# Performance work log

Measured on AMD Instinct MI355X. Metric: run time of the kernel, lower is better.

The kernel has to match this reference:

```python
import jax, jax.numpy as jnp
import numpy as np

B, S, D = 4, 2048, 512
H, DK, DV = 8, 64, 64


def setup_inputs() -> dict:
    key = jax.random.key(0)
    ks = jax.random.split(key, 9)
    inp = {
        "input_Q": jax.random.normal(ks[0], (B, S, D), dtype=jnp.float32),
        "input_K": jax.random.normal(ks[1], (B, S, D), dtype=jnp.float32),
        "input_V": jax.random.normal(ks[2], (B, S, D), dtype=jnp.float32),
        "attn_mask": jax.random.bernoulli(ks[3], 0.1, (B, S, S)),
        "other": jax.random.normal(ks[4], (B, S, S), dtype=jnp.float32),
        # nn.Linear weights stored [out_features, in_features]
        "W_Q": jax.random.normal(ks[5], (H * DK, D), dtype=jnp.float32) * (1.0 / np.sqrt(D)),
        "W_K": jax.random.normal(ks[6], (H * DK, D), dtype=jnp.float32) * (1.0 / np.sqrt(D)),
        "W_V": jax.random.normal(ks[7], (H * DV, D), dtype=jnp.float32) * (1.0 / np.sqrt(D)),
        "W_fc": jax.random.normal(ks[8], (D, H * DV), dtype=jnp.float32) * (1.0 / np.sqrt(H * DV)),
    }
    return inp


def reference(input_Q, input_K, input_V, attn_mask, other, W_Q, W_K, W_V, W_fc):
    b, s, _ = input_Q.shape
    # projections: y = x @ W.T, then split heads -> [B,H,S,dk]
    Q = (input_Q @ W_Q.T).reshape(b, s, H, DK).transpose(0, 2, 1, 3)
    K = (input_K @ W_K.T).reshape(b, s, H, DK).transpose(0, 2, 1, 3)
    V = (input_V @ W_V.T).reshape(b, s, H, DV).transpose(0, 2, 1, 3)
    scale = 1.0 / np.sqrt(DK).astype(np.float32)
    scores = jnp.einsum("bhqd,bhkd->bhqk", Q, K) * scale  # [B,H,S,S]
    scores = scores + other[:, None, :, :]  # additive bias broadcast over heads
    scores = jnp.where(attn_mask[:, None, :, :], jnp.float32(-1e9), scores)
    attn = jax.nn.softmax(scores, axis=-1)
    context = jnp.einsum("bhqk,bhkd->bhqd", attn, V)  # [B,H,S,DV]
    context = context.transpose(0, 2, 1, 3).reshape(b, s, H * DV)
    output = context @ W_fc.T  # dropout is identity at inference
    return (output, attn)
```

## Files before the change

kernel.cpp:

```cpp
#include <hip/hip_runtime.h>

#define BB 4
#define SS 2048
#define DDIM 512
#define HH 8
#define MTOK (BB*SS)
#define BHN (BB*HH)

typedef _Float16 f16;
typedef __attribute__((ext_vector_type(8))) _Float16 half8;
typedef __attribute__((ext_vector_type(4))) _Float16 half4;
typedef __attribute__((ext_vector_type(4))) float float4v;
typedef __attribute__((ext_vector_type(4))) int int4v;

#define SCALE_L2E 0.180336880073616f
#define L2E 1.44269504088896f
#define EBIAS 4.0f
#define MASKVAL -65504.0f

__device__ __forceinline__ float4v mfma_k32(half8 a, half8 b, float4v c) {
  return __builtin_amdgcn_mfma_f32_16x16x32_f16(a, b, c, 0, 0, 0);
}

__device__ __forceinline__ half8 cvt8(float4v a, float4v b) {
  half8 r;
  r[0] = (f16)a[0]; r[1] = (f16)a[1]; r[2] = (f16)a[2]; r[3] = (f16)a[3];
  r[4] = (f16)b[0]; r[5] = (f16)b[1]; r[6] = (f16)b[2]; r[7] = (f16)b[3];
  return r;
}

__global__ __launch_bounds__(256) void detect_mask_kernel(
    const unsigned int* __restrict__ m, unsigned int* __restrict__ flag) {
  unsigned int v = 0;
  const int base = blockIdx.x * 1024;
  for (int j = threadIdx.x; j < 1024; j += 256)
    if (m[base + j] > 1u) v = 1u;
  if (v) atomicOr(flag, 1u);
}

__global__ __launch_bounds__(256) void gemm_qkv(
    const float* __restrict__ inQ, const float* __restrict__ inK,
    const float* __restrict__ inV, const float* __restrict__ WQ,
    const float* __restrict__ WK, const float* __restrict__ WV,
    f16* __restrict__ Qp, f16* __restrict__ Kfrag, f16* __restrict__ Vfrag) {
  __shared__ f16 As[128][40];
  __shared__ f16 Bs[128][40];
  const int z = blockIdx.z;
  const float* A = (z == 0) ? inQ : (z == 1) ? inK : inV;
  const float* W = (z == 0) ? WQ : (z == 1) ? WK : WV;
  const int t = threadIdx.x;
  const int bm = blockIdx.x * 128;
  const int bn = blockIdx.y * 128;
  const int w = t >> 6, ln = t & 63;
  const int wr = w >> 1, wc = w & 1;
  const int lr = ln & 15, lg = ln >> 4;
  const int srow = t >> 1, scol = (t & 1) * 16;

  float4v acc[4][4] = {};

  for (int k0 = 0; k0 < 512; k0 += 32) {
    {
      const float* ap = A + (size_t)(bm + srow) * 512 + k0 + scol;
      float4v x0 = *(const float4v*)ap,       x1 = *(const float4v*)(ap + 4);
      float4v x2 = *(const float4v*)(ap + 8), x3 = *(const float4v*)(ap + 12);
      *(half8*)&As[srow][scol]     = cvt8(x0, x1);
      *(half8*)&As[srow][scol + 8] = cvt8(x2, x3);
    }
    {
      const float* wp = W + (size_t)(bn + srow) * 512 + k0 + scol;
      float4v x0 = *(const float4v*)wp,       x1 = *(const float4v*)(wp + 4);
      float4v x2 = *(const float4v*)(wp + 8), x3 = *(const float4v*)(wp + 12);
      *(half8*)&Bs[srow][scol]     = cvt8(x0, x1);
      *(half8*)&Bs[srow][scol + 8] = cvt8(x2, x3);
    }
    __syncthreads();
    half8 af[4], bf[4];
    #pragma unroll
    for (int m = 0; m < 4; m++) af[m] = *(const half8*)&As[wr * 64 + m * 16 + lr][lg * 8];
    #pragma unroll
    for (int n = 0; n < 4; n++) bf[n] = *(const half8*)&Bs[wc * 64 + n * 16 + lr][lg * 8];
    #pragma unroll
    for (int m = 0; m < 4; m++)
      #pragma unroll
      for (int n = 0; n < 4; n++) acc[m][n] = mfma_k32(af[m], bf[n], acc[m][n]);
    __syncthreads();
  }

  #pragma unroll
  for (int m = 0; m < 4; m++) {
    int row = bm + wr * 64 + m * 16 + lg * 4;
    #pragma unroll
    for (int n = 0; n < 4; n++) {
      int col = bn + wc * 64 + n * 16 + lr;
      int b_ = row >> 11, s_ = row & 2047, h_ = col >> 6, d_ = col & 63;
      if (z == 0) {
        #pragma unroll
        for (int r = 0; r < 4; r++)
          Qp[(size_t)(row + r) * 512 + col] = (f16)acc[m][n][r];
      } else if (z == 1) {
        #pragma unroll
        for (int r = 0; r < 4; r++) {
          int tok = s_ + r;
          Kfrag[((((size_t)(b_ * 8 + h_)) * 128 + (tok >> 4)) * 2 + (d_ >> 5)) * 512 +
                ((tok & 15) + 16 * ((d_ >> 3) & 3)) * 8 + (d_ & 7)] =
              (f16)acc[m][n][r];
        }
      } else {
        half4 ph;
        ph[0] = (f16)acc[m][n][0]; ph[1] = (f16)acc[m][n][1];
        ph[2] = (f16)acc[m][n][2]; ph[3] = (f16)acc[m][n][3];
        *(half4*)&Vfrag[((((size_t)(b_ * 8 + h_)) * 64 + (s_ >> 5)) * 4 + (d_ >> 4)) * 512 +
                        ((d_ & 15) + 16 * ((s_ >> 2) & 3)) * 8 + ((s_ >> 2) & 4)] = ph;
      }
    }
  }
}

__global__ __launch_bounds__(256) void gemm_out(const f16* __restrict__ ctx2,
                                                const float* __restrict__ W,
                                                float* __restrict__ Out) {
  __shared__ f16 As[128][40];
  __shared__ f16 Bs[128][40];
  const int t = threadIdx.x;
  const int bm = blockIdx.x * 128;
  const int bn = blockIdx.y * 128;
  const int w = t >> 6, ln = t & 63;
  const int wr = w >> 1, wc = w & 1;
  const int lr = ln & 15, lg = ln >> 4;
  const int srow = t >> 1, scol = (t & 1) * 16;

  float4v acc[4][4] = {};

  for (int k0 = 0; k0 < 512; k0 += 32) {
    {
      const f16* ap = ctx2 + (size_t)(bm + srow) * 512 + k0 + scol;
      const f16* ap2 = ap + (size_t)MTOK * 512;
      half8 x0 = *(const half8*)(ap),  x1 = *(const half8*)(ap + 8);
      half8 y0 = *(const half8*)(ap2), y1 = *(const half8*)(ap2 + 8);
      *(half8*)&As[srow][scol]     = x0 + y0;
      *(half8*)&As[srow][scol + 8] = x1 + y1;
    }
    {
      const float* wp = W + (size_t)(bn + srow) * 512 + k0 + scol;
      float4v x0 = *(const float4v*)wp,       x1 = *(const float4v*)(wp + 4);
      float4v x2 = *(const float4v*)(wp + 8), x3 = *(const float4v*)(wp + 12);
      *(half8*)&Bs[srow][scol]     = cvt8(x0, x1);
      *(half8*)&Bs[srow][scol + 8] = cvt8(x2, x3);
    }
    __syncthreads();
    half8 af[4], bf[4];
    #pragma unroll
    for (int m = 0; m < 4; m++) af[m] = *(const half8*)&As[wr * 64 + m * 16 + lr][lg * 8];
    #pragma unroll
    for (int n = 0; n < 4; n++) bf[n] = *(const half8*)&Bs[wc * 64 + n * 16 + lr][lg * 8];
    #pragma unroll
    for (int m = 0; m < 4; m++)
      #pragma unroll
      for (int n = 0; n < 4; n++) acc[m][n] = mfma_k32(af[m], bf[n], acc[m][n]);
    __syncthreads();
  }

  #pragma unroll
  for (int m = 0; m < 4; m++) {
    int row = bm + wr * 64 + m * 16 + lg * 4;
    #pragma unroll
    for (int n = 0; n < 4; n++) {
      int col = bn + wc * 64 + n * 16 + lr;
      #pragma unroll
      for (int r = 0; r < 4; r++)
        Out[(size_t)(row + r) * 512 + col] = acc[m][n][r];
    }
  }
}

#define LOADK(dst, st) {                                        \
    const f16* p_ = kfb + (size_t)(st) * 2048;                  \
    dst##0 = *(const half8*)(p_);                               \
    dst##1 = *(const half8*)(p_ + 512);                         \
    dst##2 = *(const half8*)(p_ + 1024);                        \
    dst##3 = *(const half8*)(p_ + 1536); }
#define LOADV(dst, st) {                                        \
    const f16* p_ = vfb + (size_t)(st) * 2048;                  \
    dst##0 = *(const half8*)(p_);                               \
    dst##1 = *(const half8*)(p_ + 512);                         \
    dst##2 = *(const half8*)(p_ + 1024);                        \
    dst##3 = *(const half8*)(p_ + 1536); }

template<int PHASE>
__global__ __launch_bounds__(512, (PHASE == 1) ? 6 : 4) void attn_pass(
    const f16* __restrict__ Qp, const f16* __restrict__ Kfrag,
    const f16* __restrict__ Vfrag, const float* __restrict__ other,
    const unsigned char* __restrict__ mask8, const int* __restrict__ mask32,
    const unsigned int* __restrict__ flag, float* __restrict__ lsum2,
    float* __restrict__ attn_out, f16* __restrict__ ctx2) {
  __shared__ f16 othm[16][1032];

  const int t = threadIdx.x;
  const int bid = blockIdx.x;
  const int b  = (bid >> 1) & 3;
  const int kh = bid & 1;
  const int qblk = (bid >> 3) * 16;
  const int w = t >> 6, ln = t & 63;
  const int lr = ln & 15, lg = ln >> 4;
  const bool use8 = (*flag) != 0;

  {
    const int q = t >> 5, k0 = (t & 31) * 32;
    const size_t base = ((size_t)b * SS + qblk + q) * SS + kh * 1024 + k0;
    const float* op = other + base;
    if (use8) {
      const unsigned char* mp = mask8 + base;
      #pragma unroll
      for (int g = 0; g < 4; g++) {
        unsigned int mw0 = *(const unsigned int*)(mp + g * 8);
        unsigned int mw1 = *(const unsigned int*)(mp + g * 8 + 4);
        float4v o0 = *(const float4v*)(op + g * 8);
        float4v o1 = *(const float4v*)(op + g * 8 + 4);
        float4v r0, r1;
        #pragma unroll
        for (int r = 0; r < 4; r++) {
          r0[r] = ((mw0 >> (8 * r)) & 0xffu) ? MASKVAL : fmaf(o0[r], L2E, -EBIAS);
          r1[r] = ((mw1 >> (8 * r)) & 0xffu) ? MASKVAL : fmaf(o1[r], L2E, -EBIAS);
        }
        *(half8*)&othm[q][k0 + g * 8] = cvt8(r0, r1);
      }
    } else {
      const int* mp = mask32 + base;
      #pragma unroll
      for (int g = 0; g < 4; g++) {
        int4v m0 = *(const int4v*)(mp + g * 8);
        int4v m1 = *(const int4v*)(mp + g * 8 + 4);
        float4v o0 = *(const float4v*)(op + g * 8);
        float4v o1 = *(const float4v*)(op + g * 8 + 4);
        float4v r0, r1;
        #pragma unroll
        for (int r = 0; r < 4; r++) {
          r0[r] = m0[r] ? MASKVAL : fmaf(o0[r], L2E, -EBIAS);
          r1[r] = m1[r] ? MASKVAL : fmaf(o1[r], L2E, -EBIAS);
        }
        *(half8*)&othm[q][k0 + g * 8] = cvt8(r0, r1);
      }
    }
  }
  __syncthreads();

  const int h = w, bh = b * 8 + h;
  const f16* qp = Qp + ((size_t)b * SS + qblk + lr) * 512 + h * 64 + lg * 8;
  const half8 qf0 = *(const half8*)qp;
  const half8 qf1 = *(const half8*)(qp + 32);

  float invl = 0.f;
  if (PHASE == 2) {
    const size_t qi = (size_t)bh * SS + qblk + lr;
    invl = 1.0f / (lsum2[qi] + lsum2[(size_t)BHN * SS + qi]);
  }

  float rs = 0.f;
  float4v cacc0 = {}, cacc1 = {}, cacc2 = {}, cacc3 = {};

  const f16* kfb = Kfrag + ((size_t)bh * 128 + kh * 64) * 2 * 512 + ln * 8;
  const f16* vfb = Vfrag + ((size_t)bh * 64 + kh * 32) * 4 * 512 + ln * 8;
  float* abase = attn_out + ((size_t)bh * SS + qblk + lr) * SS + kh * 1024;

  half8 kA0, kA1, kA2, kA3, kB0, kB1, kB2, kB3;
  half8 vA0, vA1, vA2, vA3, vB0, vB1, vB2, vB3;

  LOADK(kA, 0);
  if (PHASE == 2) LOADV(vA, 0);

  #define BODY(kf, vf, st) {                                              \
    const int stn = ((st) < 31) ? (st) + 1 : 31;                          \
    (void)stn;                                                            \
    float4v s0 = {}, s1 = {};                                             \
    s0 = mfma_k32(kf##0, qf0, s0);                                        \
    s0 = mfma_k32(kf##1, qf1, s0);                                        \
    s1 = mfma_k32(kf##2, qf0, s1);                                        \
    s1 = mfma_k32(kf##3, qf1, s1);                                        \
    const int kl = (st) * 32;                                             \
    const half4 o40 = *(const half4*)&othm[lr][kl + lg * 4];              \
    const half4 o41 = *(const half4*)&othm[lr][kl + 16 + lg * 4];         \
    float4v ev0, ev1;                                                     \
    _Pragma("unroll")                                                     \
    for (int r = 0; r < 4; r++) {                                         \
      ev0[r] = exp2f(fmaf(s0[r], SCALE_L2E, (float)o40[r]));              \
      ev1[r] = exp2f(fmaf(s1[r], SCALE_L2E, (float)o41[r]));              \
    }                                                                     \
    if (PHASE == 1) {                                                     \
      rs += (ev0[0] + ev0[1]) + (ev0[2] + ev0[3]) +                       \
            (ev1[0] + ev1[1]) + (ev1[2] + ev1[3]);                        \
    } else {                                                              \
      float4v av0 = ev0 * invl, av1 = ev1 * invl;                         \
      *(float4v*)(abase + kl + lg * 4) = av0;                             \
      *(float4v*)(abase + kl + 16 + lg * 4) = av1;                        \
      half8 pa8 = cvt8(av0, av1);                                         \
      cacc0 = mfma_k32(pa8, vf##0, cacc0);                                \
      cacc1 = mfma_k32(pa8, vf##1, cacc1);                                \
      cacc2 = mfma_k32(pa8, vf##2, cacc2);                                \
      cacc3 = mfma_k32(pa8, vf##3, cacc3);                                \
    }                                                                     \
  }

  for (int st2 = 0; st2 < 16; st2++) {
    const int se = st2 * 2;
    {
      const int stn = (se < 31) ? se + 1 : 31;
      LOADK(kB, stn);
      if (PHASE == 2) LOADV(vB, stn);
      BODY(kA, vA, se);
    }
    {
      const int so = se + 1;
      const int stn = (so < 31) ? so + 1 : 31;
      LOADK(kA, stn);
      if (PHASE == 2) LOADV(vA, stn);
      BODY(kB, vB, so);
    }
  }
  #undef BODY

  if (PHASE == 1) {
    float v = rs;
    v += __shfl_xor(v, 16);
    v += __shfl_xor(v, 32);
    if (ln < 16)
      lsum2[(size_t)kh * BHN * SS + (size_t)bh * SS + qblk + lr] = v;
  } else {
    #pragma unroll
    for (int r = 0; r < 4; r++) {
      const size_t crow = (size_t)kh * MTOK * 512 +
                          ((size_t)b * SS + qblk + lg * 4 + r) * 512 + h * 64;
      ctx2[crow + 0 * 16 + lr] = (f16)cacc0[r];
      ctx2[crow + 1 * 16 + lr] = (f16)cacc1[r];
      ctx2[crow + 2 * 16 + lr] = (f16)cacc2[r];
      ctx2[crow + 3 * 16 + lr] = (f16)cacc3[r];
    }
  }
}

extern "C" void kernel_launch(void* const* d_in, const int* in_sizes, int n_in,
                              void* d_out, int out_size, void* d_ws, size_t ws_size,
                              hipStream_t stream) {
  const float* inQ   = (const float*)d_in[0];
  const float* inK   = (const float*)d_in[1];
  const float* inV   = (const float*)d_in[2];
  const void*  mask  = d_in[3];
  const float* other = (const float*)d_in[4];
  const float* WQ    = (const float*)d_in[5];
  const float* WK    = (const float*)d_in[6];
  const float* WV    = (const float*)d_in[7];
  const float* WF    = (const float*)d_in[8];

  char* ws = (char*)d_ws;
  size_t off = 0;
  unsigned int* flag = (unsigned int*)(ws + off); off += 256;
  f16* Qp    = (f16*)(ws + off); off += (size_t)MTOK * 512 * 2;
  f16* Kfrag = (f16*)(ws + off); off += (size_t)MTOK * 512 * 2;
  f16* Vfrag = (f16*)(ws + off); off += (size_t)MTOK * 512 * 2;
  float* lsum2 = (float*)(ws + off); off += (size_t)2 * BHN * SS * 4;
  f16* ctx2  = (f16*)(ws + off); off += (size_t)2 * MTOK * 512 * 2;
  if (ws_size < off) return;

  float* outp  = (float*)d_out;
  float* attnp = outp + (size_t)MTOK * DDIM;

  hipMemsetAsync(flag, 0, 256, stream);
  detect_mask_kernel<<<64, 256, 0, stream>>>((const unsigned int*)mask, flag);

  gemm_qkv<<<dim3(64, 4, 3), 256, 0, stream>>>(inQ, inK, inV, WQ, WK, WV,
                                               Qp, Kfrag, Vfrag);

  attn_pass<1><<<1024, 512, 0, stream>>>(
      Qp, Kfrag, Vfrag, other, (const unsigned char*)mask, (const int*)mask,
      flag, lsum2, attnp, ctx2);
  attn_pass<2><<<1024, 512, 0, stream>>>(
      Qp, Kfrag, Vfrag, other, (const unsigned char*)mask, (const int*)mask,
      flag, lsum2, attnp, ctx2);

  gemm_out<<<dim3(64, 4), 256, 0, stream>>>(ctx2, WF, outp);
}
```

Baseline: 377.5 us.

## Fuse two attention passes into one kernel covering full key range per block

Replaces the two-launch attention scheme (a row-sum pass and a normalize+PV pass, each split across two key halves) with a single kernel in which each block handles all 2048 keys for a 16-query tile. The block computes the row sum and then recomputes the scores for normalization and the PV product. This removes the second read and preprocessing of the mask/bias into shared memory, the lsum2 workspace, and the half-summed ctx2 buffer that gemm_out had to add. In exchange the grid halves to 512 blocks, shared memory per block doubles, and occupancy drops (launch bounds 512,2), which may reduce latency hiding.

```diff
diff --git a/kernel.cpp b/kernel.cpp
--- a/kernel.cpp
+++ b/kernel.cpp
@@ -116,7 +116,7 @@
   }
 }
 
-__global__ __launch_bounds__(256) void gemm_out(const f16* __restrict__ ctx2,
+__global__ __launch_bounds__(256) void gemm_out(const f16* __restrict__ ctx,
                                                 const float* __restrict__ W,
                                                 float* __restrict__ Out) {
   __shared__ f16 As[128][40];
@@ -133,12 +133,9 @@
 
   for (int k0 = 0; k0 < 512; k0 += 32) {
     {
-      const f16* ap = ctx2 + (size_t)(bm + srow) * 512 + k0 + scol;
-      const f16* ap2 = ap + (size_t)MTOK * 512;
-      half8 x0 = *(const half8*)(ap),  x1 = *(const half8*)(ap + 8);
-      half8 y0 = *(const half8*)(ap2), y1 = *(const half8*)(ap2 + 8);
-      *(half8*)&As[srow][scol]     = x0 + y0;
-      *(half8*)&As[srow][scol + 8] = x1 + y1;
+      const f16* ap = ctx + (size_t)(bm + srow) * 512 + k0 + scol;
+      *(half8*)&As[srow][scol]     = *(const half8*)(ap);
+      *(half8*)&As[srow][scol + 8] = *(const half8*)(ap + 8);
     }
     {
       const float* wp = W + (size_t)(bn + srow) * 512 + k0 + scol;
@@ -186,32 +183,30 @@
     dst##2 = *(const half8*)(p_ + 1024);                        \
     dst##3 = *(const half8*)(p_ + 1536); }
 
-template<int PHASE>
-__global__ __launch_bounds__(512, (PHASE == 1) ? 6 : 4) void attn_pass(
+__global__ __launch_bounds__(512, 2) void attn_fused(
     const f16* __restrict__ Qp, const f16* __restrict__ Kfrag,
     const f16* __restrict__ Vfrag, const float* __restrict__ other,
     const unsigned char* __restrict__ mask8, const int* __restrict__ mask32,
-    const unsigned int* __restrict__ flag, float* __restrict__ lsum2,
-    float* __restrict__ attn_out, f16* __restrict__ ctx2) {
-  __shared__ f16 othm[16][1032];
+    const unsigned int* __restrict__ flag, float* __restrict__ attn_out,
+    f16* __restrict__ ctx) {
+  __shared__ f16 othm[16][2056];
 
   const int t = threadIdx.x;
   const int bid = blockIdx.x;
-  const int b  = (bid >> 1) & 3;
-  const int kh = bid & 1;
-  const int qblk = (bid >> 3) * 16;
+  const int b = bid & 3;
+  const int qblk = (bid >> 2) * 16;
   const int w = t >> 6, ln = t & 63;
   const int lr = ln & 15, lg = ln >> 4;
   const bool use8 = (*flag) != 0;
 
   {
-    const int q = t >> 5, k0 = (t & 31) * 32;
-    const size_t base = ((size_t)b * SS + qblk + q) * SS + kh * 1024 + k0;
+    const int q = t >> 5, k0 = (t & 31) * 64;
+    const size_t base = ((size_t)b * SS + qblk + q) * SS + k0;
     const float* op = other + base;
     if (use8) {
       const unsigned char* mp = mask8 + base;
       #pragma unroll
-      for (int g = 0; g < 4; g++) {
+      for (int g = 0; g < 8; g++) {
         unsigned int mw0 = *(const unsigned int*)(mp + g * 8);
         unsigned int mw1 = *(const unsigned int*)(mp + g * 8 + 4);
         float4v o0 = *(const float4v*)(op + g * 8);
@@ -227,7 +222,7 @@
     } else {
       const int* mp = mask32 + base;
       #pragma unroll
-      for (int g = 0; g < 4; g++) {
+      for (int g = 0; g < 8; g++) {
         int4v m0 = *(const int4v*)(mp + g * 8);
         int4v m1 = *(const int4v*)(mp + g * 8 + 4);
         float4v o0 = *(const float4v*)(op + g * 8);
@@ -249,28 +244,17 @@
   const half8 qf0 = *(const half8*)qp;
   const half8 qf1 = *(const half8*)(qp + 32);
 
-  float invl = 0.f;
-  if (PHASE == 2) {
-    const size_t qi = (size_t)bh * SS + qblk + lr;
-    invl = 1.0f / (lsum2[qi] + lsum2[(size_t)BHN * SS + qi]);
-  }
-
-  float rs = 0.f;
-  float4v cacc0 = {}, cacc1 = {}, cacc2 = {}, cacc3 = {};
-
-  const f16* kfb = Kfrag + ((size_t)bh * 128 + kh * 64) * 2 * 512 + ln * 8;
-  const f16* vfb = Vfrag + ((size_t)bh * 64 + kh * 32) * 4 * 512 + ln * 8;
-  float* abase = attn_out + ((size_t)bh * SS + qblk + lr) * SS + kh * 1024;
+  const f16* kfb = Kfrag + (size_t)bh * 128 * 2 * 512 + ln * 8;
+  const f16* vfb = Vfrag + (size_t)bh * 64 * 4 * 512 + ln * 8;
+  float* abase = attn_out + ((size_t)bh * SS + qblk + lr) * SS;
 
   half8 kA0, kA1, kA2, kA3, kB0, kB1, kB2, kB3;
   half8 vA0, vA1, vA2, vA3, vB0, vB1, vB2, vB3;
 
+  float rs = 0.f;
   LOADK(kA, 0);
-  if (PHASE == 2) LOADV(vA, 0);
-
-  #define BODY(kf, vf, st) {                                              \
-    const int stn = ((st) < 31) ? (st) + 1 : 31;                          \
-    (void)stn;                                                            \
+
+  #define BODYA(kf, st) {                                                 \
     float4v s0 = {}, s1 = {};                                             \
     s0 = mfma_k32(kf##0, qf0, s0);                                        \
     s0 = mfma_k32(kf##1, qf1, s0);                                        \
@@ -285,55 +269,82 @@
       ev0[r] = exp2f(fmaf(s0[r], SCALE_L2E, (float)o40[r]));              \
       ev1[r] = exp2f(fmaf(s1[r], SCALE_L2E, (float)o41[r]));              \
     }                                                                     \
-    if (PHASE == 1) {                                                     \
-      rs += (ev0[0] + ev0[1]) + (ev0[2] + ev0[3]) +                       \
-            (ev1[0] + ev1[1]) + (ev1[2] + ev1[3]);                        \
-    } else {                                                              \
-      float4v av0 = ev0 * invl, av1 = ev1 * invl;                         \
-      *(float4v*)(abase + kl + lg * 4) = av0;                             \
-      *(float4v*)(abase + kl + 16 + lg * 4) = av1;                        \
-      half8 pa8 = cvt8(av0, av1);                                         \
-      cacc0 = mfma_k32(pa8, vf##0, cacc0);                                \
-      cacc1 = mfma_k32(pa8, vf##1, cacc1);                                \
-      cacc2 = mfma_k32(pa8, vf##2, cacc2);                                \
-      cacc3 = mfma_k32(pa8, vf##3, cacc3);                                \
+    rs += (ev0[0] + ev0[1]) + (ev0[2] + ev0[3]) +                         \
+          (ev1[0] + ev1[1]) + (ev1[2] + ev1[3]);                          \
+  }
+
+  for (int st2 = 0; st2 < 32; st2++) {
+    const int se = st2 * 2;
+    {
+      LOADK(kB, se + 1);
+      BODYA(kA, se);
+    }
+    {
+      const int so = se + 1;
+      const int stn = (so < 63) ? so + 1 : 63;
+      LOADK(kA, stn);
+      BODYA(kB, so);
+    }
+  }
+  #undef BODYA
+
+  rs += __shfl_xor(rs, 16);
+  rs += __shfl_xor(rs, 32);
+  const float invl = 1.0f / rs;
+
+  float4v cacc0 = {}, cacc1 = {}, cacc2 = {}, cacc3 = {};
+  LOADK(kA, 0);
+  LOADV(vA, 0);
+
+  #define BODYB(kf, vf, st) {                                             \
+    float4v s0 = {}, s1 = {};                                             \
+    s0 = mfma_k32(kf##0, qf0, s0);                                        \
+    s0 = mfma_k32(kf##1, qf1, s0);                                        \
+    s1 = mfma_k32(kf##2, qf0, s1);                                        \
+    s1 = mfma_k32(kf##3, qf1, s1);                                        \
+    const int kl = (st) * 32;                                             \
+    const half4 o40 = *(const half4*)&othm[lr][kl + lg * 4];              \
+    const half4 o41 = *(const half4*)&othm[lr][kl + 16 + lg * 4];         \
+    float4v ev0, ev1;                                                     \
+    _Pragma("unroll")                                                     \
+    for (int r = 0; r < 4; r++) {                                         \
+      ev0[r] = exp2f(fmaf(s0[r], SCALE_L2E, (float)o40[r]));              \
+      ev1[r] = exp2f(fmaf(s1[r], SCALE_L2E, (float)o41[r]));              \
     }                                                                     \
-  }
-
-  for (int st2 = 0; st2 < 16; st2++) {
+    float4v av0 = ev0 * invl, av1 = ev1 * invl;                           \
+    *(float4v*)(abase + kl + lg * 4) = av0;                               \
+    *(float4v*)(abase + kl + 16 + lg * 4) = av1;                          \
+    half8 pa8 = cvt8(av0, av1);                                           \
+    cacc0 = mfma_k32(pa8, vf##0, cacc0);                                  \
+    cacc1 = mfma_k32(pa8, vf##1, cacc1);                                  \
+    cacc2 = mfma_k32(pa8, vf##2, cacc2);                                  \
+    cacc3 = mfma_k32(pa8, vf##3, cacc3);                                  \
+  }
+
+  for (int st2 = 0; st2 < 32; st2++) {
     const int se = st2 * 2;
     {
-      const int stn = (se < 31) ? se + 1 : 31;
-      LOADK(kB, stn);
-      if (PHASE == 2) LOADV(vB, stn);
-      BODY(kA, vA, se);
+      LOADK(kB, se + 1);
+      LOADV(vB, se + 1);
+      BODYB(kA, vA, se);
     }
     {
       const int so = se + 1;
-      const int stn = (so < 31) ? so + 1 : 31;
+      const int stn = (so < 63) ? so + 1 : 63;
       LOADK(kA, stn);
-      if (PHASE == 2) LOADV(vA, stn);
-      BODY(kB, vB, so);
-    }
-  }
-  #undef BODY
-
-  if (PHASE == 1) {
-    float v = rs;
-    v += __shfl_xor(v, 16);
-    v += __shfl_xor(v, 32);
-    if (ln < 16)
-      lsum2[(size_t)kh * BHN * SS + (size_t)bh * SS + qblk + lr] = v;
-  } else {
-    #pragma unroll
-    for (int r = 0; r < 4; r++) {
-      const size_t crow = (size_t)kh * MTOK * 512 +
-                          ((size_t)b * SS + qblk + lg * 4 + r) * 512 + h * 64;
-      ctx2[crow + 0 * 16 + lr] = (f16)cacc0[r];
-      ctx2[crow + 1 * 16 + lr] = (f16)cacc1[r];
-      ctx2[crow + 2 * 16 + lr] = (f16)cacc2[r];
-      ctx2[crow + 3 * 16 + lr] = (f16)cacc3[r];
-    }
+      LOADV(vA, stn);
+      BODYB(kB, vB, so);
+    }
+  }
+  #undef BODYB
+
+  #pragma unroll
+  for (int r = 0; r < 4; r++) {
+    const size_t crow = ((size_t)b * SS + qblk + lg * 4 + r) * 512 + h * 64;
+    ctx[crow + 0 * 16 + lr] = (f16)cacc0[r];
+    ctx[crow + 1 * 16 + lr] = (f16)cacc1[r];
+    ctx[crow + 2 * 16 + lr] = (f16)cacc2[r];
+    ctx[crow + 3 * 16 + lr] = (f16)cacc3[r];
   }
 }
 
@@ -356,8 +367,7 @@
   f16* Qp    = (f16*)(ws + off); off += (size_t)MTOK * 512 * 2;
   f16* Kfrag = (f16*)(ws + off); off += (size_t)MTOK * 512 * 2;
   f16* Vfrag = (f16*)(ws + off); off += (size_t)MTOK * 512 * 2;
-  float* lsum2 = (float*)(ws + off); off += (size_t)2 * BHN * SS * 4;
-  f16* ctx2  = (f16*)(ws + off); off += (size_t)2 * MTOK * 512 * 2;
+  f16* ctx   = (f16*)(ws + off); off += (size_t)MTOK * 512 * 2;
   if (ws_size < off) return;
 
   float* outp  = (float*)d_out;
@@ -369,12 +379,9 @@
   gemm_qkv<<<dim3(64, 4, 3), 256, 0, stream>>>(inQ, inK, inV, WQ, WK, WV,
                                                Qp, Kfrag, Vfrag);
 
-  attn_pass<1><<<1024, 512, 0, stream>>>(
+  attn_fused<<<512, 512, 0, stream>>>(
       Qp, Kfrag, Vfrag, other, (const unsigned char*)mask, (const int*)mask,
-      flag, lsum2, attnp, ctx2);
-  attn_pass<2><<<1024, 512, 0, stream>>>(
-      Qp, Kfrag, Vfrag, other, (const unsigned char*)mask, (const int*)mask,
-      flag, lsum2, attnp, ctx2);
-
-  gemm_out<<<dim3(64, 4), 256, 0, stream>>>(ctx2, WF, outp);
-}
+      flag, attnp, ctx);
+
+  gemm_out<<<dim3(64, 4), 256, 0, stream>>>(ctx, WF, outp);
+}
```

New measurement: 364.0 us. -3.6%, faster.
